# Kernel tuning notes

Hardware: AMD Instinct MI355X
Metric: run time of the kernel (lower is better)

Reference implementation:

```python
import jax, jax.numpy as jnp
import numpy as np
import math

N_HEADS = 12
HEAD_DIM = 64
D_MODEL = 768
BATCH = 2
SEQ = 2048
GRID = 46  # num_patches_per_side


def _rope_1d(x, pos, dim):
    # x: (B,S,H,dim), pos: (S,) int -> rotary embedding along last dim
    inv_freq = 1.0 / (10000.0 ** (jnp.arange(0, dim, 2, dtype=jnp.float32) / dim))  # (dim/2,)
    ang = pos.astype(jnp.float32)[:, None] * inv_freq  # (S, dim/2)
    cos = jnp.concatenate([jnp.cos(ang), jnp.cos(ang)], axis=-1)[None, :, None, :]
    sin = jnp.concatenate([jnp.sin(ang), jnp.sin(ang)], axis=-1)[None, :, None, :]
    x1, x2 = jnp.split(x, 2, axis=-1)
    rot = jnp.concatenate([-x2, x1], axis=-1)
    return x * cos.astype(x.dtype) + rot * sin.astype(x.dtype)


def _rope_2d(x, row_ids, col_ids):
    # 2D RoPE: first half of head_dim rotated by row position, second half by column position
    half = x.shape[-1] // 2
    xr = _rope_1d(x[..., :half], row_ids, half)
    xc = _rope_1d(x[..., half:], col_ids, half)
    return jnp.concatenate([xr, xc], axis=-1)


def setup_inputs() -> dict:
    key = jax.random.key(0)
    ks = jax.random.split(key, 7)
    scale = 1.0 / math.sqrt(D_MODEL)
    return {
        "x": jax.random.normal(ks[0], (BATCH, SEQ, D_MODEL), dtype=jnp.float32),
        "row_ids": jax.random.randint(ks[1], (SEQ,), 0, GRID),
        "col_ids": jax.random.randint(ks[2], (SEQ,), 0, GRID),
        "Wq": jax.random.normal(ks[3], (D_MODEL, D_MODEL), dtype=jnp.float32) * scale,
        "Wk": jax.random.normal(ks[4], (D_MODEL, D_MODEL), dtype=jnp.float32) * scale,
        "Wv": jax.random.normal(ks[5], (D_MODEL, D_MODEL), dtype=jnp.float32) * scale,
        "Wo": jax.random.normal(ks[6], (D_MODEL, D_MODEL), dtype=jnp.float32) * scale,
    }


def reference(x, row_ids, col_ids, Wq, Wk, Wv, Wo):
    B, S, _ = x.shape
    # projections (nn.Linear: y = x @ W.T)
    q = (x @ Wq.T).reshape(B, S, N_HEADS, HEAD_DIM)
    k = (x @ Wk.T).reshape(B, S, N_HEADS, HEAD_DIM)
    v = (x @ Wv.T).reshape(B, S, N_HEADS, HEAD_DIM)
    q = _rope_2d(q, row_ids, col_ids)
    k = _rope_2d(k, row_ids, col_ids)
    # (B,H,S,D)
    q = q.transpose(0, 2, 1, 3)
    k = k.transpose(0, 2, 1, 3)
    v = v.transpose(0, 2, 1, 3)
    scale = 1.0 / math.sqrt(HEAD_DIM)
    scores = jnp.einsum('bhqd,bhkd->bhqk', q, k) * scale  # (B,H,S,S)
    causal = jnp.triu(jnp.ones((S, S), dtype=bool), k=1)
    scores = jnp.where(causal, -jnp.inf, scores)
    attn = jax.nn.softmax(scores, axis=-1)
    out = jnp.einsum('bhqk,bhkd->bhqd', attn, v)
    out = out.transpose(0, 2, 1, 3).reshape(B, S, D_MODEL)
    return out @ Wo.T
```

## Files before the change

### kernel.cpp

```cpp
#include <hip/hip_runtime.h>
#include <stdint.h>
#include <stddef.h>

#define DEV __device__ __forceinline__

typedef unsigned short u16;
typedef __attribute__((ext_vector_type(8))) __bf16 bf16x8;
typedef __attribute__((ext_vector_type(4))) float f32x4;
typedef __attribute__((ext_vector_type(8))) unsigned short u16x8;
typedef __attribute__((ext_vector_type(4))) unsigned short u16x4;

DEV u16 f2bf(float f) {
  uint32_t u = __builtin_bit_cast(uint32_t, f);
  u += 0x7fffu + ((u >> 16) & 1u);
  return (u16)(u >> 16);
}
DEV float bf2f(u16 h) {
  uint32_t u = ((uint32_t)h) << 16;
  return __builtin_bit_cast(float, u);
}
DEV f32x4 mfma16(bf16x8 a, bf16x8 b, f32x4 c) {
  return __builtin_amdgcn_mfma_f32_16x16x32_bf16(a, b, c, 0, 0, 0);
}
DEV void ld_lds16(const void* g, void* l) {
  __builtin_amdgcn_global_load_lds((const __attribute__((address_space(1))) void*)g,
                                   (__attribute__((address_space(3))) void*)l, 16, 0, 0);
}

#define Q_SCALE 0.18033688011112042f

__global__ __launch_bounds__(256) void k_cvt_all(const float* __restrict__ x,
                                                 const float* __restrict__ wq,
                                                 const float* __restrict__ wk,
                                                 const float* __restrict__ wv,
                                                 const float* __restrict__ wo,
                                                 u16* __restrict__ dx,
                                                 u16* __restrict__ dqkv,
                                                 u16* __restrict__ dwo) {
  const int bid = blockIdx.x;
  const float* src;
  u16* dst;
  int off;
  if (bid < 3072) {
    src = x; dst = dx; off = bid;
  } else {
    const int t = bid - 3072;
    const int w = t / 576;
    off = t - w * 576;
    src = (w == 0) ? wq : (w == 1) ? wk : (w == 2) ? wv : wo;
    dst = (w < 3) ? (dqkv + (size_t)w * 589824) : dwo;
  }
  const int i = (off * 256 + threadIdx.x) * 4;
  const float4 f = *(const float4*)(src + i);
  u16x4 o;
  o.x = f2bf(f.x); o.y = f2bf(f.y); o.z = f2bf(f.z); o.w = f2bf(f.w);
  *(u16x4*)(dst + i) = o;
}

__global__ __launch_bounds__(256) void k_gemm_qkv(const u16* __restrict__ A,
                                                  const u16* __restrict__ B,
                                                  const int* __restrict__ row_ids,
                                                  const int* __restrict__ col_ids,
                                                  u16* __restrict__ Qh,
                                                  u16* __restrict__ Kh,
                                                  u16* __restrict__ Vt) {
  const int K = 768;
  __shared__ __align__(16) u16 sA[128 * 64];
  __shared__ __align__(16) u16 sB[128 * 64];
  __shared__ int sIds[256];
  const int tid = threadIdx.x;
  const int lane = tid & 63;
  const int wid = tid >> 6;
  const int wm = wid & 1, wn = wid >> 1;
  const int col16 = lane & 15, quad = lane >> 4;
  const int rowBase = blockIdx.y * 128;
  const int colBase = blockIdx.x * 128;
  const int seg_r = lane >> 3;
  const int seg_c = lane & 7;

  f32x4 zero; zero[0] = zero[1] = zero[2] = zero[3] = 0.0f;
  f32x4 acc[4][4];
#pragma unroll
  for (int i = 0; i < 4; ++i)
#pragma unroll
    for (int j = 0; j < 4; ++j) acc[i][j] = zero;

  for (int k0 = 0; k0 < K; k0 += 64) {
#pragma unroll
    for (int c = 0; c < 4; ++c) {
      const int seg = wid * 4 + c;
      ld_lds16(A + (size_t)(rowBase + seg * 8 + seg_r) * K + k0 + seg_c * 8, sA + seg * 512);
      ld_lds16(B + (size_t)(colBase + seg * 8 + seg_r) * K + k0 + seg_c * 8, sB + seg * 512);
    }
    __syncthreads();
#pragma unroll
    for (int kk = 0; kk < 2; ++kk) {
      bf16x8 af[4], bfr[4];
#pragma unroll
      for (int t = 0; t < 4; ++t) {
        af[t]  = *(const bf16x8*)(sA + (wm * 64 + t * 16 + col16) * 64 + kk * 32 + quad * 8);
        bfr[t] = *(const bf16x8*)(sB + (wn * 64 + t * 16 + col16) * 64 + kk * 32 + quad * 8);
      }
#pragma unroll
      for (int tm = 0; tm < 4; ++tm)
#pragma unroll
        for (int tn = 0; tn < 4; ++tn)
          acc[tm][tn] = mfma16(af[tm], bfr[tn], acc[tm][tn]);
    }
    __syncthreads();
  }

  const int bx = blockIdx.x;
  const int type = bx / 6;
  const int h = (bx % 6) * 2 + wn;
  const int bb = rowBase >> 11;
  const int s0 = rowBase & 2047;
  const size_t bh = (size_t)bb * 12 + h;

  if (type < 2) {
    if (tid < 128) {
      sIds[tid] = row_ids[s0 + tid];
      sIds[128 + tid] = col_ids[s0 + tid];
    }
    __syncthreads();
    u16* dst = (type == 0) ? Qh : Kh;
    const float scl = (type == 0) ? Q_SCALE : 1.0f;
    const float invf = exp2f(-(float)col16 * 0.8304820237218406f);
#pragma unroll
    for (int tm = 0; tm < 4; ++tm)
#pragma unroll
      for (int r = 0; r < 4; ++r) {
        const int lrow = wm * 64 + tm * 16 + quad * 4 + r;
        const float aR = (float)sIds[lrow] * invf;
        const float aC = (float)sIds[128 + lrow] * invf;
        const float cR = __cosf(aR), sR = __sinf(aR);
        const float cC = __cosf(aC), sC = __sinf(aC);
        const float x1 = acc[tm][0][r], x2 = acc[tm][1][r];
        const float x3 = acc[tm][2][r], x4 = acc[tm][3][r];
        const float y1 = (x1 * cR - x2 * sR) * scl;
        const float y2 = (x2 * cR + x1 * sR) * scl;
        const float y3 = (x3 * cC - x4 * sC) * scl;
        const float y4 = (x4 * cC + x3 * sC) * scl;
        u16* p = dst + (bh * 2048 + s0 + lrow) * 64;
        *(uint32_t*)(p + 2 * col16)      = (uint32_t)f2bf(y1) | ((uint32_t)f2bf(y2) << 16);
        *(uint32_t*)(p + 32 + 2 * col16) = (uint32_t)f2bf(y3) | ((uint32_t)f2bf(y4) << 16);
      }
  } else {
#pragma unroll
    for (int tm = 0; tm < 4; ++tm)
#pragma unroll
      for (int tn = 0; tn < 4; ++tn) {
        const int d = tn * 16 + col16;
        const int srow = s0 + wm * 64 + tm * 16 + quad * 4;
        u16x4 o4;
#pragma unroll
        for (int r = 0; r < 4; ++r) o4[r] = f2bf(acc[tm][tn][r]);
        *(u16x4*)(Vt + (bh * 64 + d) * 2048 + srow) = o4;
      }
  }
}

__global__ __launch_bounds__(256, 3) void k_gemm_o(const u16* __restrict__ A,
                                                   const u16* __restrict__ B,
                                                   float* __restrict__ C,
                                                   int N, int K) {
  __shared__ __align__(16) u16 sA[64 * 72];
  __shared__ __align__(16) u16 sB[64 * 72];
  const int tid = threadIdx.x;
  const int lane = tid & 63;
  const int wid = tid >> 6;
  const int col16 = lane & 15, quad = lane >> 4;
  const int wm = wid & 1, wn = wid >> 1;
  const int rowBase = blockIdx.y * 64;
  const int colBase = blockIdx.x * 64;
  const int sr = tid >> 3;
  const int sc8 = (tid & 7) * 8;

  f32x4 zero; zero[0] = zero[1] = zero[2] = zero[3] = 0.0f;
  f32x4 acc[2][2];
  acc[0][0] = zero; acc[0][1] = zero; acc[1][0] = zero; acc[1][1] = zero;

  u16x8 ar[2], br[2];
  auto gload = [&](int k0) {
    ar[0] = *(const u16x8*)(A + (size_t)(rowBase + sr) * K + k0 + sc8);
    ar[1] = *(const u16x8*)(A + (size_t)(rowBase + 32 + sr) * K + k0 + sc8);
    br[0] = *(const u16x8*)(B + (size_t)(colBase + sr) * K + k0 + sc8);
    br[1] = *(const u16x8*)(B + (size_t)(colBase + 32 + sr) * K + k0 + sc8);
  };

  gload(0);
  for (int k0 = 0; k0 < K; k0 += 64) {
    __syncthreads();
    *(u16x8*)&sA[sr * 72 + sc8] = ar[0];
    *(u16x8*)&sA[(32 + sr) * 72 + sc8] = ar[1];
    *(u16x8*)&sB[sr * 72 + sc8] = br[0];
    *(u16x8*)&sB[(32 + sr) * 72 + sc8] = br[1];
    if (k0 + 64 < K) gload(k0 + 64);
    __syncthreads();
#pragma unroll
    for (int kk = 0; kk < 2; ++kk) {
      bf16x8 af[2], bfr[2];
#pragma unroll
      for (int t = 0; t < 2; ++t) {
        af[t]  = *(const bf16x8*)&sA[(wm * 32 + t * 16 + col16) * 72 + kk * 32 + quad * 8];
        bfr[t] = *(const bf16x8*)&sB[(wn * 32 + t * 16 + col16) * 72 + kk * 32 + quad * 8];
      }
#pragma unroll
      for (int tm = 0; tm < 2; ++tm)
#pragma unroll
        for (int tn = 0; tn < 2; ++tn)
          acc[tm][tn] = mfma16(af[tm], bfr[tn], acc[tm][tn]);
    }
  }

#pragma unroll
  for (int tm = 0; tm < 2; ++tm)
#pragma unroll
    for (int tn = 0; tn < 2; ++tn)
#pragma unroll
      for (int r = 0; r < 4; ++r) {
        const int row = rowBase + wm * 32 + tm * 16 + quad * 4 + r;
        const int col = colBase + wn * 32 + tn * 16 + col16;
        C[(size_t)row * N + col] = acc[tm][tn][r];
      }
}

__global__ __launch_bounds__(256, 3) void k_attn(const u16* __restrict__ Qh,
                                                 const u16* __restrict__ Kh,
                                                 const u16* __restrict__ Vt,
                                                 u16* __restrict__ O,
                                                 u16* __restrict__ Opart,
                                                 float* __restrict__ ml) {
  __shared__ __align__(16) u16 sK[2][64 * 72];
  __shared__ __align__(16) u16 sV[2][64 * 72];
  __shared__ __align__(16) u16 sP[4][16 * 72];
  const int tid = threadIdx.x;
  const int lane = tid & 63;
  const int wid = tid >> 6;
  const int col16 = lane & 15;
  const int quad = lane >> 4;
  const int bx = blockIdx.x;
  const int bh = bx / 80;
  const int u = bx - bh * 80;
  int qt, c;
  if (u < 8)       { qt = u; c = 0; }
  else if (u < 24) { const int t = u - 8;  qt = 8 + (t >> 1); c = t & 1; }
  else if (u < 48) { const int t = u - 24; const int q3 = t / 3; qt = 16 + q3; c = t - q3 * 3; }
  else             { const int t = u - 48; qt = 24 + (t >> 2); c = t & 3; }
  const int nc = (qt >> 3) + 1;
  const int tile0 = c * 8;
  const int tileE = min(tile0 + 8, qt + 1);
  const int ntiles = tileE - tile0;
  const int b = bh / 12, h = bh % 12;
  const int qw = qt * 64 + wid * 16;

  const u16* Qb = Qh + (size_t)bh * (2048 * 64);
  const u16* Kb = Kh + (size_t)bh * (2048 * 64);
  const u16* Vb = Vt + (size_t)bh * (64 * 2048);

  const bf16x8 bQ0 = *(const bf16x8*)(Qb + (size_t)(qw + col16) * 64 + quad * 8);
  const bf16x8 bQ1 = *(const bf16x8*)(Qb + (size_t)(qw + col16) * 64 + 32 + quad * 8);

  f32x4 zero; zero[0] = zero[1] = zero[2] = zero[3] = 0.0f;
  f32x4 o[4];
#pragma unroll
  for (int i = 0; i < 4; ++i) o[i] = zero;
  float m_r = -1e30f, l_r = 0.0f;

  u16* sPw = &sP[wid][0];

  const int sr = tid >> 3;
  const int sc8 = (tid & 7) * 8;
  u16x8 kr[2], vr[2];
  auto gload = [&](int kt) {
#pragma unroll
    for (int i = 0; i < 2; ++i) {
      kr[i] = *(const u16x8*)(Kb + (size_t)(kt + sr + i * 32) * 64 + sc8);
      vr[i] = *(const u16x8*)(Vb + (size_t)(sr + i * 32) * 2048 + kt + sc8);
    }
  };
  auto lwrite = [&](int buf) {
#pragma unroll
    for (int i = 0; i < 2; ++i) {
      *(u16x8*)&sK[buf][(sr + i * 32) * 72 + sc8] = kr[i];
      *(u16x8*)&sV[buf][(sr + i * 32) * 72 + sc8] = vr[i];
    }
  };

  gload(tile0 * 64);
  lwrite(0);
  if (ntiles > 1) gload((tile0 + 1) * 64);
  __syncthreads();

  for (int ki = 0; ki < ntiles; ++ki) {
    const int buf = ki & 1;
    const int kt = (tile0 + ki) * 64;
    if (ki + 1 < ntiles) {
      lwrite(buf ^ 1);
      if (ki + 2 < ntiles) gload((tile0 + ki + 2) * 64);
    }
    bf16x8 ka0[4], ka1[4];
#pragma unroll
    for (int tn = 0; tn < 4; ++tn) {
      const int base = (tn * 16 + col16) * 72 + quad * 8;
      ka0[tn] = *(const bf16x8*)&sK[buf][base];
      ka1[tn] = *(const bf16x8*)&sK[buf][base + 32];
    }
    f32x4 sc[4];
#pragma unroll
    for (int tn = 0; tn < 4; ++tn)
      sc[tn] = mfma16(ka1[tn], bQ1, mfma16(ka0[tn], bQ0, zero));
    bf16x8 va0[4], va1[4];
#pragma unroll
    for (int tn = 0; tn < 4; ++tn) {
      const int base = (tn * 16 + col16) * 72 + quad * 8;
      va0[tn] = *(const bf16x8*)&sV[buf][base];
      va1[tn] = *(const bf16x8*)&sV[buf][base + 32];
    }
    if (kt + 63 > qw) {
#pragma unroll
      for (int tn = 0; tn < 4; ++tn)
#pragma unroll
        for (int rr = 0; rr < 4; ++rr)
          if (kt + tn * 16 + quad * 4 + rr > qw + col16) sc[tn][rr] = -1e30f;
    }
    float vm = sc[0][0];
#pragma unroll
    for (int tn = 0; tn < 4; ++tn)
#pragma unroll
      for (int rr = 0; rr < 4; ++rr) vm = fmaxf(vm, sc[tn][rr]);
    vm = fmaxf(vm, __shfl_xor(vm, 16, 64));
    vm = fmaxf(vm, __shfl_xor(vm, 32, 64));
    if (__any(vm > m_r)) {
      const float mn = fmaxf(m_r, vm);
      const float alpha = exp2f(m_r - mn);
      m_r = mn;
      l_r *= alpha;
#pragma unroll
      for (int t = 0; t < 4; ++t)
#pragma unroll
        for (int rr = 0; rr < 4; ++rr) o[t][rr] *= alpha;
    }
    const float mn = m_r;
    float rs = 0.0f;
#pragma unroll
    for (int tn = 0; tn < 4; ++tn)
#pragma unroll
      for (int h2 = 0; h2 < 2; ++h2) {
        const float p0 = exp2f(sc[tn][2 * h2] - mn);
        const float p1 = exp2f(sc[tn][2 * h2 + 1] - mn);
        rs += p0 + p1;
        const uint32_t w = (uint32_t)f2bf(p0) | ((uint32_t)f2bf(p1) << 16);
        ((uint32_t*)sPw)[col16 * 36 + tn * 8 + quad * 2 + h2] = w;
      }
    rs += __shfl_xor(rs, 16, 64);
    rs += __shfl_xor(rs, 32, 64);
    l_r += rs;
    asm volatile("s_waitcnt lgkmcnt(0)" ::: "memory");
    const bf16x8 bP0 = *(const bf16x8*)(sPw + col16 * 72 + quad * 8);
    const bf16x8 bP1 = *(const bf16x8*)(sPw + col16 * 72 + 32 + quad * 8);
#pragma unroll
    for (int tn = 0; tn < 4; ++tn)
      o[tn] = mfma16(va1[tn], bP1, mfma16(va0[tn], bP0, o[tn]));
    __syncthreads();
  }

  if (nc == 1) {
    const float invl = 1.0f / l_r;
    const size_t row = (size_t)b * 2048 + qw + col16;
#pragma unroll
    for (int tn = 0; tn < 4; ++tn)
#pragma unroll
      for (int h2 = 0; h2 < 2; ++h2) {
        const float v0 = o[tn][2 * h2] * invl;
        const float v1 = o[tn][2 * h2 + 1] * invl;
        const uint32_t w = (uint32_t)f2bf(v0) | ((uint32_t)f2bf(v1) << 16);
        const int col = h * 64 + tn * 16 + quad * 4 + 2 * h2;
        *(uint32_t*)(O + row * 768 + col) = w;
      }
  } else {
    u16* op = Opart + (size_t)bx * 4096 + (wid * 16 + col16) * 64;
#pragma unroll
    for (int tn = 0; tn < 4; ++tn)
#pragma unroll
      for (int h2 = 0; h2 < 2; ++h2) {
        const uint32_t w = (uint32_t)f2bf(o[tn][2 * h2]) | ((uint32_t)f2bf(o[tn][2 * h2 + 1]) << 16);
        *(uint32_t*)(op + tn * 16 + quad * 4 + 2 * h2) = w;
      }
    if (quad == 0) {
      float* mlp = ml + (size_t)bx * 128;
      mlp[wid * 16 + col16] = m_r;
      mlp[64 + wid * 16 + col16] = l_r;
    }
  }
}

__global__ __launch_bounds__(256) void k_combine(const u16* __restrict__ Opart,
                                                 const float* __restrict__ ml,
                                                 u16* __restrict__ O) {
  const int bx = blockIdx.x;
  const int bh = bx / 24;
  const int qt = 8 + (bx - bh * 24);
  const int b = bh / 12, h = bh % 12;
  const int nc = (qt >> 3) + 1;
  const int prefix = (qt < 16) ? (8 + 2 * (qt - 8))
                   : (qt < 24) ? (24 + 3 * (qt - 16))
                               : (48 + 4 * (qt - 24));
  const int slot0 = bh * 80 + prefix;
  const int tid = threadIdx.x;
  const int r = tid >> 2;
  const int d0 = (tid & 3) * 16;

  float m_i[4], w_i[4];
  float M = -1e30f;
  for (int i = 0; i < nc; ++i) {
    m_i[i] = ml[(size_t)(slot0 + i) * 128 + r];
    M = fmaxf(M, m_i[i]);
  }
  float l = 0.0f;
  for (int i = 0; i < nc; ++i) {
    w_i[i] = exp2f(m_i[i] - M);
    l += w_i[i] * ml[(size_t)(slot0 + i) * 128 + 64 + r];
  }
  const float invl = 1.0f / l;

  float a[16];
#pragma unroll
  for (int j = 0; j < 16; ++j) a[j] = 0.0f;
  for (int i = 0; i < nc; ++i) {
    const u16* op = Opart + (size_t)(slot0 + i) * 4096 + r * 64 + d0;
    const u16x8 v0 = *(const u16x8*)op;
    const u16x8 v1 = *(const u16x8*)(op + 8);
#pragma unroll
    for (int j = 0; j < 8; ++j) {
      a[j] += w_i[i] * bf2f(v0[j]);
      a[8 + j] += w_i[i] * bf2f(v1[j]);
    }
  }
  u16x8 o0, o1;
#pragma unroll
  for (int j = 0; j < 8; ++j) {
    o0[j] = f2bf(a[j] * invl);
    o1[j] = f2bf(a[8 + j] * invl);
  }
  u16* dst = O + (size_t)(b * 2048 + qt * 64 + r) * 768 + h * 64 + d0;
  *(u16x8*)dst = o0;
  *(u16x8*)(dst + 8) = o1;
}

extern "C" void kernel_launch(void* const* d_in, const int* in_sizes, int n_in,
                              void* d_out, int out_size, void* d_ws, size_t ws_size,
                              hipStream_t stream) {
  const float* x       = (const float*)d_in[0];
  const int*   row_ids = (const int*)d_in[1];
  const int*   col_ids = (const int*)d_in[2];
  const float* Wq      = (const float*)d_in[3];
  const float* Wk      = (const float*)d_in[4];
  const float* Wv      = (const float*)d_in[5];
  const float* Wo      = (const float*)d_in[6];
  float* out = (float*)d_out;

  uint8_t* w8 = (uint8_t*)d_ws;
  u16* x_bf = (u16*)(w8 + 0);
  u16* wqkv = (u16*)(w8 + 6291456);
  u16* wo   = (u16*)(w8 + 9830400);
  u16* qh   = (u16*)(w8 + 29884416);
  u16* kh   = (u16*)(w8 + 36175872);
  u16* vt   = (u16*)(w8 + 42467328);
  u16* obuf = (u16*)(w8 + 48758784);
  u16*   opart = (u16*)(w8 + 11010048);
  float* mlbuf = (float*)(w8 + 11010048 + 15728640);

  k_cvt_all<<<5376, 256, 0, stream>>>(x, Wq, Wk, Wv, Wo, x_bf, wqkv, wo);
  k_gemm_qkv<<<dim3(18, 32), 256, 0, stream>>>(x_bf, wqkv, row_ids, col_ids, qh, kh, vt);
  k_attn<<<1920, 256, 0, stream>>>(qh, kh, vt, obuf, opart, mlbuf);
  k_combine<<<576, 256, 0, stream>>>(opart, mlbuf, obuf);
  k_gemm_o<<<dim3(12, 64), 256, 0, stream>>>(obuf, wo, out, 768, 768);
}
```

Measured before the change: 186.9 us.

## Widen conversion, retile output GEMM with direct-to-LDS loads, drop branchy softmax rescale

The conversion kernel now handles eight elements per thread with 16-byte stores, which halves the block count. The output projection GEMM switches to 64x128 tiles that load straight into LDS through global_load_lds, with no register prefetch and no padding, and declares an occupancy hint of 4. The attention kernel replaces the wave-uniform conditional rescale with an unconditional alpha rescale of the accumulators on every tile, trading the branch and vote for extra multiplies. The unpadded LDS layout may cause bank conflicts, and the GEMM loses its register-level double buffering.

```diff
diff --git a/kernel.cpp b/kernel.cpp
--- a/kernel.cpp
+++ b/kernel.cpp
@@ -41,20 +41,22 @@
   const float* src;
   u16* dst;
   int off;
-  if (bid < 3072) {
+  if (bid < 1536) {
     src = x; dst = dx; off = bid;
   } else {
-    const int t = bid - 3072;
-    const int w = t / 576;
-    off = t - w * 576;
+    const int t = bid - 1536;
+    const int w = t / 288;
+    off = t - w * 288;
     src = (w == 0) ? wq : (w == 1) ? wk : (w == 2) ? wv : wo;
     dst = (w < 3) ? (dqkv + (size_t)w * 589824) : dwo;
   }
-  const int i = (off * 256 + threadIdx.x) * 4;
-  const float4 f = *(const float4*)(src + i);
-  u16x4 o;
-  o.x = f2bf(f.x); o.y = f2bf(f.y); o.z = f2bf(f.z); o.w = f2bf(f.w);
-  *(u16x4*)(dst + i) = o;
+  const int i = (off * 256 + threadIdx.x) * 8;
+  const float4 f0 = *(const float4*)(src + i);
+  const float4 f1 = *(const float4*)(src + i + 4);
+  u16x8 o;
+  o[0] = f2bf(f0.x); o[1] = f2bf(f0.y); o[2] = f2bf(f0.z); o[3] = f2bf(f0.w);
+  o[4] = f2bf(f1.x); o[5] = f2bf(f1.y); o[6] = f2bf(f1.z); o[7] = f2bf(f1.w);
+  *(u16x8*)(dst + i) = o;
 }
 
 __global__ __launch_bounds__(256) void k_gemm_qkv(const u16* __restrict__ A,
@@ -160,67 +162,64 @@
   }
 }
 
-__global__ __launch_bounds__(256, 3) void k_gemm_o(const u16* __restrict__ A,
+__global__ __launch_bounds__(256, 4) void k_gemm64(const u16* __restrict__ A,
                                                    const u16* __restrict__ B,
                                                    float* __restrict__ C,
                                                    int N, int K) {
-  __shared__ __align__(16) u16 sA[64 * 72];
-  __shared__ __align__(16) u16 sB[64 * 72];
+  __shared__ __align__(16) u16 sA[64 * 64];
+  __shared__ __align__(16) u16 sB[128 * 64];
   const int tid = threadIdx.x;
   const int lane = tid & 63;
   const int wid = tid >> 6;
   const int col16 = lane & 15, quad = lane >> 4;
-  const int wm = wid & 1, wn = wid >> 1;
   const int rowBase = blockIdx.y * 64;
-  const int colBase = blockIdx.x * 64;
-  const int sr = tid >> 3;
-  const int sc8 = (tid & 7) * 8;
+  const int colBase = blockIdx.x * 128;
+  const int seg_r = lane >> 3;
+  const int seg_c = lane & 7;
 
   f32x4 zero; zero[0] = zero[1] = zero[2] = zero[3] = 0.0f;
-  f32x4 acc[2][2];
-  acc[0][0] = zero; acc[0][1] = zero; acc[1][0] = zero; acc[1][1] = zero;
-
-  u16x8 ar[2], br[2];
-  auto gload = [&](int k0) {
-    ar[0] = *(const u16x8*)(A + (size_t)(rowBase + sr) * K + k0 + sc8);
-    ar[1] = *(const u16x8*)(A + (size_t)(rowBase + 32 + sr) * K + k0 + sc8);
-    br[0] = *(const u16x8*)(B + (size_t)(colBase + sr) * K + k0 + sc8);
-    br[1] = *(const u16x8*)(B + (size_t)(colBase + 32 + sr) * K + k0 + sc8);
-  };
-
-  gload(0);
+  f32x4 acc[4][2];
+#pragma unroll
+  for (int i = 0; i < 4; ++i) { acc[i][0] = zero; acc[i][1] = zero; }
+
   for (int k0 = 0; k0 < K; k0 += 64) {
-    __syncthreads();
-    *(u16x8*)&sA[sr * 72 + sc8] = ar[0];
-    *(u16x8*)&sA[(32 + sr) * 72 + sc8] = ar[1];
-    *(u16x8*)&sB[sr * 72 + sc8] = br[0];
-    *(u16x8*)&sB[(32 + sr) * 72 + sc8] = br[1];
-    if (k0 + 64 < K) gload(k0 + 64);
+#pragma unroll
+    for (int c = 0; c < 2; ++c) {
+      const int seg = wid * 2 + c;
+      ld_lds16(A + (size_t)(rowBase + seg * 8 + seg_r) * K + k0 + seg_c * 8, sA + seg * 512);
+    }
+#pragma unroll
+    for (int c = 0; c < 4; ++c) {
+      const int seg = wid * 4 + c;
+      ld_lds16(B + (size_t)(colBase + seg * 8 + seg_r) * K + k0 + seg_c * 8, sB + seg * 512);
+    }
     __syncthreads();
 #pragma unroll
     for (int kk = 0; kk < 2; ++kk) {
-      bf16x8 af[2], bfr[2];
-#pragma unroll
-      for (int t = 0; t < 2; ++t) {
-        af[t]  = *(const bf16x8*)&sA[(wm * 32 + t * 16 + col16) * 72 + kk * 32 + quad * 8];
-        bfr[t] = *(const bf16x8*)&sB[(wn * 32 + t * 16 + col16) * 72 + kk * 32 + quad * 8];
-      }
-#pragma unroll
-      for (int tm = 0; tm < 2; ++tm)
+      bf16x8 af[4], bfr[2];
+#pragma unroll
+      for (int t = 0; t < 4; ++t)
+        af[t] = *(const bf16x8*)(sA + (t * 16 + col16) * 64 + kk * 32 + quad * 8);
+#pragma unroll
+      for (int t = 0; t < 2; ++t)
+        bfr[t] = *(const bf16x8*)(sB + (wid * 32 + t * 16 + col16) * 64 + kk * 32 + quad * 8);
+#pragma unroll
+      for (int tm = 0; tm < 4; ++tm)
 #pragma unroll
         for (int tn = 0; tn < 2; ++tn)
           acc[tm][tn] = mfma16(af[tm], bfr[tn], acc[tm][tn]);
     }
-  }
-
-#pragma unroll
-  for (int tm = 0; tm < 2; ++tm)
+    __syncthreads();
+  }
+
+#pragma unroll
+  for (int tm = 0; tm < 4; ++tm)
 #pragma unroll
     for (int tn = 0; tn < 2; ++tn)
 #pragma unroll
       for (int r = 0; r < 4; ++r) {
-        const int row = rowBase + wm * 32 + tm * 16 + quad * 4 + r;
-        const int col = colBase + wn * 32 + tn * 16 + col16;
+        const int row = rowBase + tm * 16 + quad * 4 + r;
+        const int col = colBase + wid * 32 + tn * 16 + col16;
         C[(size_t)row * N + col] = acc[tm][tn][r];
       }
 }
@@ -331,17 +330,9 @@
       for (int rr = 0; rr < 4; ++rr) vm = fmaxf(vm, sc[tn][rr]);
     vm = fmaxf(vm, __shfl_xor(vm, 16, 64));
     vm = fmaxf(vm, __shfl_xor(vm, 32, 64));
-    if (__any(vm > m_r)) {
-      const float mn = fmaxf(m_r, vm);
-      const float alpha = exp2f(m_r - mn);
-      m_r = mn;
-      l_r *= alpha;
-#pragma unroll
-      for (int t = 0; t < 4; ++t)
-#pragma unroll
-        for (int rr = 0; rr < 4; ++rr) o[t][rr] *= alpha;
-    }
-    const float mn = m_r;
+    const float mn = fmaxf(m_r, vm);
+    const float alpha = exp2f(m_r - mn);
+    m_r = mn;
     float rs = 0.0f;
 #pragma unroll
     for (int tn = 0; tn < 4; ++tn)
@@ -355,7 +346,11 @@
       }
     rs += __shfl_xor(rs, 16, 64);
     rs += __shfl_xor(rs, 32, 64);
-    l_r += rs;
+    l_r = l_r * alpha + rs;
+#pragma unroll
+    for (int t = 0; t < 4; ++t)
+#pragma unroll
+      for (int rr = 0; rr < 4; ++rr) o[t][rr] *= alpha;
     asm volatile("s_waitcnt lgkmcnt(0)" ::: "memory");
     const bf16x8 bP0 = *(const bf16x8*)(sPw + col16 * 72 + quad * 8);
     const bf16x8 bP1 = *(const bf16x8*)(sPw + col16 * 72 + 32 + quad * 8);
@@ -471,9 +466,9 @@
   u16*   opart = (u16*)(w8 + 11010048);
   float* mlbuf = (float*)(w8 + 11010048 + 15728640);
 
-  k_cvt_all<<<5376, 256, 0, stream>>>(x, Wq, Wk, Wv, Wo, x_bf, wqkv, wo);
+  k_cvt_all<<<2688, 256, 0, stream>>>(x, Wq, Wk, Wv, Wo, x_bf, wqkv, wo);
   k_gemm_qkv<<<dim3(18, 32), 256, 0, stream>>>(x_bf, wqkv, row_ids, col_ids, qh, kh, vt);
   k_attn<<<1920, 256, 0, stream>>>(qh, kh, vt, obuf, opart, mlbuf);
   k_combine<<<576, 256, 0, stream>>>(opart, mlbuf, obuf);
-  k_gemm_o<<<dim3(12, 64), 256, 0, stream>>>(obuf, wo, out, 768, 768);
-}
+  k_gemm64<<<dim3(6, 64), 256, 0, stream>>>(obuf, wo, out, 768, 768);
+}
```

Result: no change. 188.3 us (+0.7%).
